# Performance work log

Hardware: AMD Instinct MI355X
Metric: run time of the kernel (lower is better)

Reference implementation:

```python
import jax, jax.numpy as jnp
import numpy as np

N, E = 100000, 1600000
IN_C, HID_C, OUT_C = 128, 64, 40


def setup_inputs() -> dict:
    key = jax.random.key(0)
    ks = jax.random.split(key, 8)
    s = lambda fan_in: 1.0 / np.sqrt(fan_in)
    return {
        "x": jax.random.normal(ks[0], (N, IN_C), dtype=jnp.float32),
        "edge_index": jax.random.randint(ks[1], (2, E), 0, N, dtype=jnp.int64),
        # SAGEConv layer 1: lin_l (on aggregated neighbors, with bias) + lin_r (root, no bias)
        "W_l1": jax.random.uniform(ks[2], (IN_C, HID_C), jnp.float32, -s(IN_C), s(IN_C)),
        "b_l1": jnp.zeros((HID_C,), jnp.float32),
        "W_r1": jax.random.uniform(ks[3], (IN_C, HID_C), jnp.float32, -s(IN_C), s(IN_C)),
        # SAGEConv layer 2
        "W_l2": jax.random.uniform(ks[4], (HID_C, OUT_C), jnp.float32, -s(HID_C), s(HID_C)),
        "b_l2": jnp.zeros((OUT_C,), jnp.float32),
        "W_r2": jax.random.uniform(ks[5], (HID_C, OUT_C), jnp.float32, -s(HID_C), s(HID_C)),
    }


def _sage_conv(x, src, dst, W_l, b_l, W_r, n_nodes):
    # mean-aggregate neighbor features: scatter-add x[src] onto dst, divide by degree
    agg = jax.ops.segment_sum(x[src], dst, num_segments=n_nodes)  # [N, F]
    deg = jax.ops.segment_sum(jnp.ones((src.shape[0],), x.dtype), dst, num_segments=n_nodes)
    mean = agg / jnp.maximum(deg, 1.0)[:, None]
    return mean @ W_l + b_l + x @ W_r


def reference(x, edge_index, W_l1, b_l1, W_r1, W_l2, b_l2, W_r2):
    src, dst = edge_index[0], edge_index[1]  # messages flow src -> dst
    # eval mode: dropout is identity
    hid = _sage_conv(x, src, dst, W_l1, b_l1, W_r1, N)
    hid = jax.nn.relu(hid)
    out = _sage_conv(hid, src, dst, W_l2, b_l2, W_r2, N)
    return jax.nn.log_softmax(out, axis=1)
```

## Files before the change

kernel.cpp:

```cpp
#include <hip/hip_runtime.h>
#include <hip/hip_bf16.h>

#define N_NODES 100000
#define E_EDGES 1600000
#define IN_C 128
#define HID_C 64
#define OUT_C 40

#define NBUCK 196
#define BCAP 9216
#define B1_EPT 16
#define B1_CHUNK (256 * B1_EPT)
#define B1_GRID ((E_EDGES + B1_CHUNK - 1) / B1_CHUNK)
#define TILE_GRID ((N_NODES + 63) / 64)

typedef unsigned short ushort_t;
typedef unsigned int uint_t;
typedef unsigned char uchar_t;
typedef __attribute__((ext_vector_type(8))) short bf16x8;
typedef __attribute__((ext_vector_type(4))) float f32x4;
typedef __attribute__((ext_vector_type(2))) float f32x2;

__device__ __forceinline__ float bfu2f(ushort_t u) {
    return __uint_as_float(((uint_t)u) << 16);
}
__device__ __forceinline__ ushort_t f2bfu(float f) {
    uint_t u = __float_as_uint(f);
    return (ushort_t)((u + 0x7FFFu + ((u >> 16) & 1u)) >> 16);
}
__device__ __forceinline__ uchar_t f2fp8(float f) {
    int p = __builtin_amdgcn_cvt_pk_fp8_f32(f, f, 0, false);
    return (uchar_t)(p & 0xff);
}

__global__ __launch_bounds__(256) void k_prep(const int* __restrict__ src, const int* __restrict__ dst,
                                              int* __restrict__ bcur, int* __restrict__ bucket,
                                              const float* __restrict__ Wl1, const float* __restrict__ Wr1,
                                              const float* __restrict__ Wl2, const float* __restrict__ Wr2,
                                              ushort_t* __restrict__ Wt1, ushort_t* __restrict__ Wt2) {
    __shared__ int cnt[NBUCK];
    __shared__ int base[NBUCK];
    const int t = threadIdx.x;

    if (blockIdx.x < B1_GRID) {
        const int e0 = blockIdx.x * B1_CHUNK;
        for (int i = t; i < NBUCK; i += 256) cnt[i] = 0;
        __syncthreads();

        int myp[B1_EPT];
        int myb[B1_EPT];
#pragma unroll
        for (int j = 0; j < B1_EPT; ++j) {
            int e = e0 + t + j * 256;
            if (e < E_EDGES) {
                int d = dst[e];
                myp[j] = src[e] | ((d & 511) << 17);
                myb[j] = d >> 9;
                atomicAdd(&cnt[myb[j]], 1);
            } else {
                myb[j] = -1;
            }
        }
        __syncthreads();
        for (int i = t; i < NBUCK; i += 256) {
            base[i] = atomicAdd(&bcur[i], cnt[i]);
            cnt[i] = 0;
        }
        __syncthreads();
#pragma unroll
        for (int j = 0; j < B1_EPT; ++j) {
            if (myb[j] >= 0) {
                int b = myb[j];
                int loc = atomicAdd(&cnt[b], 1);
                int pos = base[b] + loc;
                if (pos < BCAP) bucket[(size_t)b * BCAP + pos] = myp[j];
            }
        }
    } else {
        int i = (blockIdx.x - B1_GRID) * 256 + t;
        if (i < 128 * 128) {
            int n = i >> 7, k = i & 127;
            float v = (n < 64) ? Wl1[k * 64 + n] : Wr1[k * 64 + (n - 64)];
            Wt1[n * 128 + k] = f2bfu(v);
        }
        if (i < 80 * 64) {
            int n = i >> 6, k = i & 63;
            float v = (n < 40) ? Wl2[k * 40 + n] : Wr2[k * 40 + (n - 40)];
            Wt2[n * 64 + k] = f2bfu(v);
        }
    }
}

struct SmemCsr {
    int red[256];
    int hist[512];
    int sc[2][512];
    int cur[512];
    int csrbuf[BCAP];
};
struct SmemGemm1 {
    ushort_t xs[64 * 136];
    ushort_t wsm[128 * 136];
};
union SmemK2 {
    SmemCsr c;
    SmemGemm1 g;
};

__global__ __launch_bounds__(256) void k_csr_gemm1(const int* __restrict__ bucket, const int* __restrict__ bcur,
                                                   int* __restrict__ rowptr, int* __restrict__ csr,
                                                   const float* __restrict__ x, const ushort_t* __restrict__ Wt,
                                                   uchar_t* __restrict__ h1l, ushort_t* __restrict__ h1r) {
    __shared__ SmemK2 sm;
    const int t = threadIdx.x;

    if (blockIdx.x < NBUCK) {
        const int b = blockIdx.x;
        const int n0 = b << 9;
        const int nb = min(512, N_NODES - n0);
        const int sz = min(bcur[b], BCAP);
        const int* bdata = bucket + (size_t)b * BCAP;

        int v = (t < b) ? min(bcur[t], BCAP) : 0;
        sm.c.red[t] = v;
        __syncthreads();
        for (int off = 128; off > 0; off >>= 1) {
            if (t < off) sm.c.red[t] += sm.c.red[t + off];
            __syncthreads();
        }
        const int cbase = sm.c.red[0];

        for (int i = t; i < 512; i += 256) sm.c.hist[i] = 0;
        __syncthreads();
        for (int i = t; i < sz; i += 256) {
            int p = bdata[i];
            atomicAdd(&sm.c.hist[p >> 17], 1);
        }
        __syncthreads();
        for (int i = t; i < 512; i += 256) sm.c.sc[0][i] = sm.c.hist[i];
        __syncthreads();
        int pp = 0;
        for (int off = 1; off < 512; off <<= 1) {
            for (int i = t; i < 512; i += 256)
                sm.c.sc[1 - pp][i] = sm.c.sc[pp][i] + ((i >= off) ? sm.c.sc[pp][i - off] : 0);
            __syncthreads();
            pp ^= 1;
        }
        for (int i = t; i < 512; i += 256) {
            int exc = sm.c.sc[pp][i] - sm.c.hist[i];
            sm.c.cur[i] = exc;
            if (i < nb) rowptr[n0 + i] = cbase + exc;
        }
        __syncthreads();
        for (int i = t; i < sz; i += 256) {
            int p = bdata[i];
            int pos = atomicAdd(&sm.c.cur[p >> 17], 1);
            sm.c.csrbuf[pos] = (p & 0x1FFFF) << 6;
        }
        __syncthreads();
        for (int i = t; i < sz; i += 256)
            csr[cbase + i] = sm.c.csrbuf[i];
        if (b == NBUCK - 1 && t == 0) rowptr[N_NODES] = cbase + sz;
    } else {
        const int row_base = (blockIdx.x - NBUCK) * 64;

        for (int i = t; i < 128 * 16; i += 256) {
            int n = i >> 4, seg = i & 15;
            uint4 v = *(const uint4*)(Wt + n * 128 + seg * 8);
            *(uint4*)(sm.g.wsm + n * 136 + seg * 8) = v;
        }
        for (int i = t; i < 64 * 32; i += 256) {
            int row = i >> 5, seg = i & 31;
            int gr = row_base + row;
            float4 v = make_float4(0.f, 0.f, 0.f, 0.f);
            if (gr < N_NODES) v = *(const float4*)(x + (size_t)gr * IN_C + seg * 4);
            ushort4 u;
            u.x = f2bfu(v.x); u.y = f2bfu(v.y); u.z = f2bfu(v.z); u.w = f2bfu(v.w);
            *(ushort4*)(sm.g.xs + row * 136 + seg * 4) = u;
        }
        __syncthreads();

        const int wv = t >> 6, lane = t & 63;
        const int m = lane & 15, quad = lane >> 4;
        const int m0 = wv * 16;

        bf16x8 a[4];
#pragma unroll
        for (int kk = 0; kk < 4; ++kk)
            a[kk] = *(const bf16x8*)(sm.g.xs + (m0 + m) * 136 + kk * 32 + quad * 8);

        f32x4 acc[8];
#pragma unroll
        for (int nt = 0; nt < 8; ++nt) acc[nt] = (f32x4){0.f, 0.f, 0.f, 0.f};

#pragma unroll
        for (int nt = 0; nt < 8; ++nt) {
#pragma unroll
            for (int kk = 0; kk < 4; ++kk) {
                bf16x8 b = *(const bf16x8*)(sm.g.wsm + (nt * 16 + m) * 136 + kk * 32 + quad * 8);
                acc[nt] = __builtin_amdgcn_mfma_f32_16x16x32_bf16(a[kk], b, acc[nt], 0, 0, 0);
            }
        }

        const int grow_base = row_base + m0 + quad * 4;
#pragma unroll
        for (int r = 0; r < 4; ++r) {
            int grow = grow_base + r;
            if (grow < N_NODES) {
#pragma unroll
                for (int nt = 0; nt < 4; ++nt)
                    h1l[(size_t)grow * HID_C + nt * 16 + m] = f2fp8(acc[nt][r]);
#pragma unroll
                for (int nt = 4; nt < 8; ++nt)
                    h1r[(size_t)grow * HID_C + (nt - 4) * 16 + m] = f2bfu(acc[nt][r]);
            }
        }
    }
}

__global__ __launch_bounds__(256) void k_agg1_gemm2(const int* __restrict__ rowptr, const int* __restrict__ csr,
                                                    const uchar_t* __restrict__ h1l, const ushort_t* __restrict__ h1r,
                                                    const float* __restrict__ b1, const ushort_t* __restrict__ Wt,
                                                    uchar_t* __restrict__ h2l, ushort_t* __restrict__ h2r) {
    __shared__ ushort_t hs[64 * 72];
    __shared__ ushort_t wsm[80 * 72];
    const int t = threadIdx.x;
    const int row_base = blockIdx.x * 64;
    const int wv = t >> 6, lane = t & 63;
    const int slot = lane >> 3;
    const int part = lane & 7;

    for (int i = t; i < 80 * 8; i += 256) {
        int n = i >> 3, seg = i & 7;
        uint4 v = *(const uint4*)(Wt + n * 64 + seg * 8);
        *(uint4*)(wsm + n * 72 + seg * 8) = v;
    }

    float4 bb0, bb1;
    if (slot == 0) {
        bb0 = *(const float4*)(b1 + part * 8);
        bb1 = *(const float4*)(b1 + part * 8 + 4);
    }
    for (int r16 = 0; r16 < 16; ++r16) {
        int lrow = wv * 16 + r16;
        int row = row_base + lrow;
        if (row < N_NODES) {
            int2 rp = *(const int2*)(rowptr + row);
            int start = rp.x, end = rp.y;
            f32x2 acc[4];
#pragma unroll
            for (int j = 0; j < 4; ++j) acc[j] = (f32x2){0.f, 0.f};

            int base = start;
            for (; base + 8 <= end; base += 8) {
                int s = csr[base + slot];
                uint2 u = *(const uint2*)(h1l + s + part * 8);
                acc[0] += __builtin_amdgcn_cvt_pk_f32_fp8(u.x, false);
                acc[1] += __builtin_amdgcn_cvt_pk_f32_fp8(u.x, true);
                acc[2] += __builtin_amdgcn_cvt_pk_f32_fp8(u.y, false);
                acc[3] += __builtin_amdgcn_cvt_pk_f32_fp8(u.y, true);
            }
            if (base < end) {
                int e = base + slot;
                int s = csr[min(e, end - 1)];
                uint2 u = *(const uint2*)(h1l + s + part * 8);
                if (e >= end) { u.x = 0u; u.y = 0u; }
                acc[0] += __builtin_amdgcn_cvt_pk_f32_fp8(u.x, false);
                acc[1] += __builtin_amdgcn_cvt_pk_f32_fp8(u.x, true);
                acc[2] += __builtin_amdgcn_cvt_pk_f32_fp8(u.y, false);
                acc[3] += __builtin_amdgcn_cvt_pk_f32_fp8(u.y, true);
            }
#pragma unroll
            for (int off = 8; off <= 32; off <<= 1) {
#pragma unroll
                for (int j = 0; j < 4; ++j) {
                    f32x2 tt;
                    tt.x = __shfl_xor(acc[j].x, off);
                    tt.y = __shfl_xor(acc[j].y, off);
                    acc[j] += tt;
                }
            }
            if (slot == 0) {
                float inv = __builtin_amdgcn_rcpf(fmaxf((float)(end - start), 1.0f));
                ushort_t rr[8];
                *(uint4*)rr = *(const uint4*)(h1r + (size_t)row * HID_C + part * 8);
                ushort_t o[8];
                o[0] = f2bfu(fmaxf(acc[0].x * inv + bfu2f(rr[0]) + bb0.x, 0.f));
                o[1] = f2bfu(fmaxf(acc[0].y * inv + bfu2f(rr[1]) + bb0.y, 0.f));
                o[2] = f2bfu(fmaxf(acc[1].x * inv + bfu2f(rr[2]) + bb0.z, 0.f));
                o[3] = f2bfu(fmaxf(acc[1].y * inv + bfu2f(rr[3]) + bb0.w, 0.f));
                o[4] = f2bfu(fmaxf(acc[2].x * inv + bfu2f(rr[4]) + bb1.x, 0.f));
                o[5] = f2bfu(fmaxf(acc[2].y * inv + bfu2f(rr[5]) + bb1.y, 0.f));
                o[6] = f2bfu(fmaxf(acc[3].x * inv + bfu2f(rr[6]) + bb1.z, 0.f));
                o[7] = f2bfu(fmaxf(acc[3].y * inv + bfu2f(rr[7]) + bb1.w, 0.f));
                *(uint4*)(hs + lrow * 72 + part * 8) = *(const uint4*)o;
            }
        } else if (slot == 0) {
            uint4 z = make_uint4(0u, 0u, 0u, 0u);
            *(uint4*)(hs + lrow * 72 + part * 8) = z;
        }
    }
    __syncthreads();

    const int m = lane & 15, quad = lane >> 4;
    const int m0 = wv * 16;

    bf16x8 a[2];
#pragma unroll
    for (int kk = 0; kk < 2; ++kk)
        a[kk] = *(const bf16x8*)(hs + (m0 + m) * 72 + kk * 32 + quad * 8);

    f32x4 acc[5];
#pragma unroll
    for (int nt = 0; nt < 5; ++nt) acc[nt] = (f32x4){0.f, 0.f, 0.f, 0.f};

#pragma unroll
    for (int nt = 0; nt < 5; ++nt) {
#pragma unroll
        for (int kk = 0; kk < 2; ++kk) {
            bf16x8 b = *(const bf16x8*)(wsm + (nt * 16 + m) * 72 + kk * 32 + quad * 8);
            acc[nt] = __builtin_amdgcn_mfma_f32_16x16x32_bf16(a[kk], b, acc[nt], 0, 0, 0);
        }
    }

    const int grow_base = row_base + m0 + quad * 4;
#pragma unroll
    for (int r = 0; r < 4; ++r) {
        int grow = grow_base + r;
        if (grow < N_NODES) {
#pragma unroll
            for (int nt = 0; nt < 5; ++nt) {
                int col = nt * 16 + m;
                float v = acc[nt][r];
                if (col < OUT_C) h2l[(size_t)grow * 64 + col] = f2fp8(v);
                else             h2r[(size_t)grow * OUT_C + (col - OUT_C)] = f2bfu(v);
            }
        }
    }
}

__global__ __launch_bounds__(256) void k_agg2(const int* __restrict__ rowptr, const int* __restrict__ csr,
                                              const uchar_t* __restrict__ h2l, const ushort_t* __restrict__ h2r,
                                              const float* __restrict__ b2, float* __restrict__ out) {
    int row = (blockIdx.x * 256 + threadIdx.x) >> 6;
    int lane = threadIdx.x & 63;
    if (row >= N_NODES) return;
    int2 rp = *(const int2*)(rowptr + row);
    int start = rp.x, end = rp.y;
    const int slot = lane >> 3;
    const int part = lane & 7;
    f32x2 acc[4];
#pragma unroll
    for (int j = 0; j < 4; ++j) acc[j] = (f32x2){0.f, 0.f};

    int base = start;
    for (; base + 8 <= end; base += 8) {
        int s = csr[base + slot];
        uint2 u = *(const uint2*)(h2l + s + part * 8);
        acc[0] += __builtin_amdgcn_cvt_pk_f32_fp8(u.x, false);
        acc[1] += __builtin_amdgcn_cvt_pk_f32_fp8(u.x, true);
        acc[2] += __builtin_amdgcn_cvt_pk_f32_fp8(u.y, false);
        acc[3] += __builtin_amdgcn_cvt_pk_f32_fp8(u.y, true);
    }
    if (base < end) {
        int e = base + slot;
        int s = csr[min(e, end - 1)];
        uint2 u = *(const uint2*)(h2l + s + part * 8);
        if (e >= end) { u.x = 0u; u.y = 0u; }
        acc[0] += __builtin_amdgcn_cvt_pk_f32_fp8(u.x, false);
        acc[1] += __builtin_amdgcn_cvt_pk_f32_fp8(u.x, true);
        acc[2] += __builtin_amdgcn_cvt_pk_f32_fp8(u.y, false);
        acc[3] += __builtin_amdgcn_cvt_pk_f32_fp8(u.y, true);
    }
#pragma unroll
    for (int off = 8; off <= 32; off <<= 1) {
#pragma unroll
        for (int j = 0; j < 4; ++j) {
            f32x2 tt;
            tt.x = __shfl_xor(acc[j].x, off);
            tt.y = __shfl_xor(acc[j].y, off);
            acc[j] += tt;
        }
    }

    const bool fin = (slot == 0) && (part < 5);
    float inv = __builtin_amdgcn_rcpf(fmaxf((float)(end - start), 1.0f));
    f32x2 v2[4];
    if (fin) {
        size_t bi = (size_t)row * OUT_C + part * 8;
        ushort_t rr[8];
        *(uint2*)&rr[0] = *(const uint2*)(h2r + bi);
        *(uint2*)&rr[4] = *(const uint2*)(h2r + bi + 4);
        float4 bb0 = *(const float4*)(b2 + part * 8);
        float4 bb1 = *(const float4*)(b2 + part * 8 + 4);
        v2[0] = (f32x2){acc[0].x * inv + bfu2f(rr[0]) + bb0.x, acc[0].y * inv + bfu2f(rr[1]) + bb0.y};
        v2[1] = (f32x2){acc[1].x * inv + bfu2f(rr[2]) + bb0.z, acc[1].y * inv + bfu2f(rr[3]) + bb0.w};
        v2[2] = (f32x2){acc[2].x * inv + bfu2f(rr[4]) + bb1.x, acc[2].y * inv + bfu2f(rr[5]) + bb1.y};
        v2[3] = (f32x2){acc[3].x * inv + bfu2f(rr[6]) + bb1.z, acc[3].y * inv + bfu2f(rr[7]) + bb1.w};
    } else {
#pragma unroll
        for (int j = 0; j < 4; ++j) v2[j] = (f32x2){-1e30f, -1e30f};
    }
    f32x2 m2;
    m2.x = fmaxf(fmaxf(v2[0].x, v2[1].x), fmaxf(v2[2].x, v2[3].x));
    m2.y = fmaxf(fmaxf(v2[0].y, v2[1].y), fmaxf(v2[2].y, v2[3].y));
    float pm = fmaxf(m2.x, m2.y);
#pragma unroll
    for (int off = 1; off <= 4; off <<= 1) pm = fmaxf(pm, __shfl_xor(pm, off));
    float es = 0.f;
#pragma unroll
    for (int j = 0; j < 4; ++j) {
        es += __expf(v2[j].x - pm);
        es += __expf(v2[j].y - pm);
    }
#pragma unroll
    for (int off = 1; off <= 4; off <<= 1) es += __shfl_xor(es, off);
    float ls = __logf(es);
    if (fin) {
        size_t bo = (size_t)row * OUT_C + part * 8;
        *(float4*)(out + bo) = make_float4(v2[0].x - pm - ls, v2[0].y - pm - ls,
                                           v2[1].x - pm - ls, v2[1].y - pm - ls);
        *(float4*)(out + bo + 4) = make_float4(v2[2].x - pm - ls, v2[2].y - pm - ls,
                                               v2[3].x - pm - ls, v2[3].y - pm - ls);
    }
}

extern "C" void kernel_launch(void* const* d_in, const int* in_sizes, int n_in,
                              void* d_out, int out_size, void* d_ws, size_t ws_size,
                              hipStream_t stream) {
    const float* x   = (const float*)d_in[0];
    const int*   ei  = (const int*)d_in[1];
    const float* Wl1 = (const float*)d_in[2];
    const float* b1  = (const float*)d_in[3];
    const float* Wr1 = (const float*)d_in[4];
    const float* Wl2 = (const float*)d_in[5];
    const float* b2  = (const float*)d_in[6];
    const float* Wr2 = (const float*)d_in[7];

    size_t u = 0;
    int*      bucket = (int*)d_ws;             u += (size_t)NBUCK * BCAP;
    int*      bcur   = (int*)d_ws + u;         u += NBUCK + 4;
    int*      rowptr = (int*)d_ws + u;         u += N_NODES + 1;
    int*      csr    = (int*)d_ws + u;         u += E_EDGES;
    u = (u + 3) & ~(size_t)3;
    ushort_t* Wt1    = (ushort_t*)((int*)d_ws + u); u += 128 * 128 / 2;
    ushort_t* Wt2    = (ushort_t*)((int*)d_ws + u); u += 80 * 64 / 2;
    uchar_t*  h1l    = (uchar_t*)((int*)d_ws + u);  u += (size_t)N_NODES * HID_C / 4;
    ushort_t* h1r    = (ushort_t*)((int*)d_ws + u); u += (size_t)N_NODES * HID_C / 2;
    uchar_t*  h2l    = (uchar_t*)((int*)d_ws + u);  u += (size_t)N_NODES * 64 / 4;
    ushort_t* h2r    = (ushort_t*)((int*)d_ws + u); u += (size_t)N_NODES * OUT_C / 2;
    if (ws_size < u * 4) return;

    hipMemsetAsync(bcur, 0, NBUCK * sizeof(int), stream);

    const int* src = ei;
    const int* dst = ei + E_EDGES;

    k_prep<<<B1_GRID + 64, 256, 0, stream>>>(src, dst, bcur, bucket, Wl1, Wr1, Wl2, Wr2, Wt1, Wt2);
    k_csr_gemm1<<<NBUCK + TILE_GRID, 256, 0, stream>>>(bucket, bcur, rowptr, csr, x, Wt1, h1l, h1r);
    k_agg1_gemm2<<<TILE_GRID, 256, 0, stream>>>(rowptr, csr, h1l, h1r, b1, Wt2, h2l, h2r);
    k_agg2<<<N_NODES / 4, 256, 0, stream>>>(rowptr, csr, h2l, h2r, b2, (float*)d_out);
}
```

Measured before the change: 256.9 us.

## Fuse GEMM1 into edge bucketing kernel and split CSR build into own kernel

Moves the layer-1 GEMM (x times combined W) into the edge-bucketing kernel as extra blocks, so it runs alongside bucketing rather than alongside CSR construction. Each GEMM block now transposes and converts W1 to bf16 itself in shared memory, which removes the separate Wt1 buffer. The CSR build moves to its own 512-thread kernel with a single-buffer scan, and the Wt2 conversion rides along in it. In exchange, each GEMM tile redundantly converts the weights with strided fp32 reads, and the shared-memory union makes the bucketing blocks reserve the large GEMM footprint, which may lower their occupancy.

```diff
diff --git a/kernel.cpp b/kernel.cpp
--- a/kernel.cpp
+++ b/kernel.cpp
@@ -33,18 +33,30 @@
     return (uchar_t)(p & 0xff);
 }
 
-__global__ __launch_bounds__(256) void k_prep(const int* __restrict__ src, const int* __restrict__ dst,
-                                              int* __restrict__ bcur, int* __restrict__ bucket,
-                                              const float* __restrict__ Wl1, const float* __restrict__ Wr1,
-                                              const float* __restrict__ Wl2, const float* __restrict__ Wr2,
-                                              ushort_t* __restrict__ Wt1, ushort_t* __restrict__ Wt2) {
-    __shared__ int cnt[NBUCK];
-    __shared__ int base[NBUCK];
+struct SmemPrep {
+    int cnt[NBUCK];
+    int base[NBUCK];
+};
+struct SmemGemm1 {
+    ushort_t xs[64 * 136];
+    ushort_t wsm[128 * 136];
+};
+union SmemK1 {
+    SmemPrep p;
+    SmemGemm1 g;
+};
+
+__global__ __launch_bounds__(256) void k_prep_gemm1(const int* __restrict__ src, const int* __restrict__ dst,
+                                                    int* __restrict__ bcur, int* __restrict__ bucket,
+                                                    const float* __restrict__ Wl1, const float* __restrict__ Wr1,
+                                                    const float* __restrict__ x,
+                                                    uchar_t* __restrict__ h1l, ushort_t* __restrict__ h1r) {
+    __shared__ SmemK1 sm;
     const int t = threadIdx.x;
 
     if (blockIdx.x < B1_GRID) {
         const int e0 = blockIdx.x * B1_CHUNK;
-        for (int i = t; i < NBUCK; i += 256) cnt[i] = 0;
+        for (int i = t; i < NBUCK; i += 256) sm.p.cnt[i] = 0;
         __syncthreads();
 
         int myp[B1_EPT];
@@ -56,118 +68,37 @@
                 int d = dst[e];
                 myp[j] = src[e] | ((d & 511) << 17);
                 myb[j] = d >> 9;
-                atomicAdd(&cnt[myb[j]], 1);
+                atomicAdd(&sm.p.cnt[myb[j]], 1);
             } else {
                 myb[j] = -1;
             }
         }
         __syncthreads();
         for (int i = t; i < NBUCK; i += 256) {
-            base[i] = atomicAdd(&bcur[i], cnt[i]);
-            cnt[i] = 0;
+            sm.p.base[i] = atomicAdd(&bcur[i], sm.p.cnt[i]);
+            sm.p.cnt[i] = 0;
         }
         __syncthreads();
 #pragma unroll
         for (int j = 0; j < B1_EPT; ++j) {
             if (myb[j] >= 0) {
                 int b = myb[j];
-                int loc = atomicAdd(&cnt[b], 1);
-                int pos = base[b] + loc;
+                int loc = atomicAdd(&sm.p.cnt[b], 1);
+                int pos = sm.p.base[b] + loc;
                 if (pos < BCAP) bucket[(size_t)b * BCAP + pos] = myp[j];
             }
         }
     } else {
-        int i = (blockIdx.x - B1_GRID) * 256 + t;
-        if (i < 128 * 128) {
-            int n = i >> 7, k = i & 127;
-            float v = (n < 64) ? Wl1[k * 64 + n] : Wr1[k * 64 + (n - 64)];
-            Wt1[n * 128 + k] = f2bfu(v);
-        }
-        if (i < 80 * 64) {
-            int n = i >> 6, k = i & 63;
-            float v = (n < 40) ? Wl2[k * 40 + n] : Wr2[k * 40 + (n - 40)];
-            Wt2[n * 64 + k] = f2bfu(v);
-        }
-    }
-}
-
-struct SmemCsr {
-    int red[256];
-    int hist[512];
-    int sc[2][512];
-    int cur[512];
-    int csrbuf[BCAP];
-};
-struct SmemGemm1 {
-    ushort_t xs[64 * 136];
-    ushort_t wsm[128 * 136];
-};
-union SmemK2 {
-    SmemCsr c;
-    SmemGemm1 g;
-};
-
-__global__ __launch_bounds__(256) void k_csr_gemm1(const int* __restrict__ bucket, const int* __restrict__ bcur,
-                                                   int* __restrict__ rowptr, int* __restrict__ csr,
-                                                   const float* __restrict__ x, const ushort_t* __restrict__ Wt,
-                                                   uchar_t* __restrict__ h1l, ushort_t* __restrict__ h1r) {
-    __shared__ SmemK2 sm;
-    const int t = threadIdx.x;
-
-    if (blockIdx.x < NBUCK) {
-        const int b = blockIdx.x;
-        const int n0 = b << 9;
-        const int nb = min(512, N_NODES - n0);
-        const int sz = min(bcur[b], BCAP);
-        const int* bdata = bucket + (size_t)b * BCAP;
-
-        int v = (t < b) ? min(bcur[t], BCAP) : 0;
-        sm.c.red[t] = v;
-        __syncthreads();
-        for (int off = 128; off > 0; off >>= 1) {
-            if (t < off) sm.c.red[t] += sm.c.red[t + off];
-            __syncthreads();
-        }
-        const int cbase = sm.c.red[0];
-
-        for (int i = t; i < 512; i += 256) sm.c.hist[i] = 0;
-        __syncthreads();
-        for (int i = t; i < sz; i += 256) {
-            int p = bdata[i];
-            atomicAdd(&sm.c.hist[p >> 17], 1);
-        }
-        __syncthreads();
-        for (int i = t; i < 512; i += 256) sm.c.sc[0][i] = sm.c.hist[i];
-        __syncthreads();
-        int pp = 0;
-        for (int off = 1; off < 512; off <<= 1) {
-            for (int i = t; i < 512; i += 256)
-                sm.c.sc[1 - pp][i] = sm.c.sc[pp][i] + ((i >= off) ? sm.c.sc[pp][i - off] : 0);
-            __syncthreads();
-            pp ^= 1;
-        }
-        for (int i = t; i < 512; i += 256) {
-            int exc = sm.c.sc[pp][i] - sm.c.hist[i];
-            sm.c.cur[i] = exc;
-            if (i < nb) rowptr[n0 + i] = cbase + exc;
-        }
-        __syncthreads();
-        for (int i = t; i < sz; i += 256) {
-            int p = bdata[i];
-            int pos = atomicAdd(&sm.c.cur[p >> 17], 1);
-            sm.c.csrbuf[pos] = (p & 0x1FFFF) << 6;
-        }
-        __syncthreads();
-        for (int i = t; i < sz; i += 256)
-            csr[cbase + i] = sm.c.csrbuf[i];
-        if (b == NBUCK - 1 && t == 0) rowptr[N_NODES] = cbase + sz;
-    } else {
-        const int row_base = (blockIdx.x - NBUCK) * 64;
-
-        for (int i = t; i < 128 * 16; i += 256) {
-            int n = i >> 4, seg = i & 15;
-            uint4 v = *(const uint4*)(Wt + n * 128 + seg * 8);
-            *(uint4*)(sm.g.wsm + n * 136 + seg * 8) = v;
+        const int row_base = (blockIdx.x - B1_GRID) * 64;
+
+        for (int i = t; i < 128 * 64; i += 256) {
+            int n = i & 127, kp = i >> 7;
+            const float* W = (n < 64) ? Wl1 : Wr1;
+            int nn = n & 63;
+            float va = W[(2 * kp) * 64 + nn];
+            float vb = W[(2 * kp + 1) * 64 + nn];
+            uint_t u = (uint_t)f2bfu(va) | ((uint_t)f2bfu(vb) << 16);
+            *(uint_t*)(sm.g.wsm + n * 136 + 2 * kp) = u;
         }
         for (int i = t; i < 64 * 32; i += 256) {
             int row = i >> 5, seg = i & 31;
@@ -216,6 +147,71 @@
             }
         }
     }
+}
+
+__global__ __launch_bounds__(512) void k_csr(const int* __restrict__ bucket, const int* __restrict__ bcur,
+                                             int* __restrict__ rowptr, int* __restrict__ csr,
+                                             const float* __restrict__ Wl2, const float* __restrict__ Wr2,
+                                             ushort_t* __restrict__ Wt2) {
+    const int t = threadIdx.x;
+    if (blockIdx.x >= NBUCK) {
+        int i = (blockIdx.x - NBUCK) * 512 + t;
+        if (i < 80 * 64) {
+            int n = i >> 6, k = i & 63;
+            float v = (n < 40) ? Wl2[k * 40 + n] : Wr2[k * 40 + (n - 40)];
+            Wt2[n * 64 + k] = f2bfu(v);
+        }
+        return;
+    }
+
+    __shared__ int red[512];
+    __shared__ int hist[512];
+    __shared__ int scan[512];
+    __shared__ int cur[512];
+    __shared__ int csrbuf[BCAP];
+
+    const int b = blockIdx.x;
+    const int n0 = b << 9;
+    const int nb = min(512, N_NODES - n0);
+    const int sz = min(bcur[b], BCAP);
+    const int* bdata = bucket + (size_t)b * BCAP;
+
+    red[t] = (t < b) ? min(bcur[t], BCAP) : 0;
+    __syncthreads();
+    for (int off = 256; off > 0; off >>= 1) {
+        if (t < off) red[t] += red[t + off];
+        __syncthreads();
+    }
+    const int cbase = red[0];
+
+    hist[t] = 0;
+    __syncthreads();
+    for (int i = t; i < sz; i += 512) atomicAdd(&hist[bdata[i] >> 17], 1);
+    __syncthreads();
+
+    scan[t] = hist[t];
+    __syncthreads();
+    for (int off = 1; off < 512; off <<= 1) {
+        int add = (t >= off) ? scan[t - off] : 0;
+        __syncthreads();
+        scan[t] += add;
+        __syncthreads();
+    }
+
+    int exc = scan[t] - hist[t];
+    cur[t] = exc;
+    if (t < nb) rowptr[n0 + t] = cbase + exc;
+    __syncthreads();
+
+    for (int i = t; i < sz; i += 512) {
+        int p = bdata[i];
+        int pos = atomicAdd(&cur[p >> 17], 1);
+        csrbuf[pos] = (p & 0x1FFFF) << 6;
+    }
+    __syncthreads();
+    for (int i = t; i < sz; i += 512)
+        csr[cbase + i] = csrbuf[i];
+    if (b == NBUCK - 1 && t == 0) rowptr[N_NODES] = cbase + sz;
 }
 
 __global__ __launch_bounds__(256) void k_agg1_gemm2(const int* __restrict__ rowptr, const int* __restrict__ csr,
@@ -443,7 +439,6 @@
     int*      rowptr = (int*)d_ws + u;         u += N_NODES + 1;
     int*      csr    = (int*)d_ws + u;         u += E_EDGES;
     u = (u + 3) & ~(size_t)3;
-    ushort_t* Wt1    = (ushort_t*)((int*)d_ws + u); u += 128 * 128 / 2;
     ushort_t* Wt2    = (ushort_t*)((int*)d_ws + u); u += 80 * 64 / 2;
     uchar_t*  h1l    = (uchar_t*)((int*)d_ws + u);  u += (size_t)N_NODES * HID_C / 4;
     ushort_t* h1r    = (ushort_t*)((int*)d_ws + u); u += (size_t)N_NODES * HID_C / 2;
@@ -456,8 +451,8 @@
     const int* src = ei;
     const int* dst = ei + E_EDGES;
 
-    k_prep<<<B1_GRID + 64, 256, 0, stream>>>(src, dst, bcur, bucket, Wl1, Wr1, Wl2, Wr2, Wt1, Wt2);
-    k_csr_gemm1<<<NBUCK + TILE_GRID, 256, 0, stream>>>(bucket, bcur, rowptr, csr, x, Wt1, h1l, h1r);
+    k_prep_gemm1<<<B1_GRID + TILE_GRID, 256, 0, stream>>>(src, dst, bcur, bucket, Wl1, Wr1, x, h1l, h1r);
+    k_csr<<<NBUCK + 10, 512, 0, stream>>>(bucket, bcur, rowptr, csr, Wl2, Wr2, Wt2);
     k_agg1_gemm2<<<TILE_GRID, 256, 0, stream>>>(rowptr, csr, h1l, h1r, b1, Wt2, h2l, h2r);
     k_agg2<<<N_NODES / 4, 256, 0, stream>>>(rowptr, csr, h2l, h2r, b2, (float*)d_out);
 }
```

Measured after the change: 264.6 us. +3.0%, slower.
